# Performance work log

Measured on AMD Instinct MI355X. Metric: run time of the kernel, lower is better.

The kernel has to match this reference:

```python
import jax, jax.numpy as jnp
import numpy as np

DIM = 2048
HEADS = 16
HEAD_DIM = DIM // HEADS
B, S = 2, 2048


def setup_inputs() -> dict:
    key = jax.random.key(0)
    k1, k2, k3 = jax.random.split(key, 3)
    x = jax.random.normal(k1, (B, S, DIM), dtype=jnp.float32)
    # causal mask (True = keep), realistic production usage of masked_fill(mask==0,...)
    mask = jnp.tril(jnp.ones((S, S), dtype=bool))
    scale = 1.0 / np.sqrt(DIM)
    W_qkv = jax.random.normal(k2, (DIM, 3 * DIM), dtype=jnp.float32) * scale
    b_qkv = jnp.zeros((3 * DIM,), dtype=jnp.float32)
    W_out = jax.random.normal(k3, (DIM, DIM), dtype=jnp.float32) * scale
    b_out = jnp.zeros((DIM,), dtype=jnp.float32)
    return {"x": x, "mask": mask, "W_qkv": W_qkv, "b_qkv": b_qkv,
            "W_out": W_out, "b_out": b_out}


def reference(x, mask, W_qkv, b_qkv, W_out, b_out):
    b, s, d = x.shape
    # fused QKV projection: [b,s,3d]
    qkv = jnp.einsum('bsd,de->bse', x, W_qkv) + b_qkv
    # [b, s, h, 3*hd] -> [b, h, s, 3*hd] -> chunk into q,k,v
    qkv = qkv.reshape(b, s, HEADS, 3 * HEAD_DIM).transpose(0, 2, 1, 3)
    q, k, v = jnp.split(qkv, 3, axis=-1)  # each [b,h,s,hd]
    scores = jnp.einsum('bhqd,bhkd->bhqk', q, k) / np.sqrt(HEAD_DIM)
    scores = jnp.where(mask, scores, jnp.float32(-1e9))
    attn = jax.nn.softmax(scores, axis=-1)
    # dropout_rate = 0.0 (eval) -> identity
    out = jnp.einsum('bhqk,bhkd->bhqd', attn, v)  # [b,h,s,hd]
    out = out.transpose(0, 2, 1, 3).reshape(b, s, d)
    return jnp.einsum('bsd,de->bse', out, W_out) + b_out
```

## Files before the change

### kernel.cpp

```cpp
#include <hip/hip_runtime.h>
#include <hip/hip_bf16.h>

#define SEQ   2048
#define DIMSZ 2048
#define NHEAD 16
#define HD    128
#define KDIM  2048

typedef __attribute__((ext_vector_type(8))) short bf16x8;
typedef __attribute__((ext_vector_type(4))) float f32x4;
typedef __attribute__((ext_vector_type(4))) short short4v;
typedef __attribute__((ext_vector_type(4))) float float4v;

__device__ __forceinline__ short f2bf(float f) {
    union { __hip_bfloat16 h; short s; } u;
    u.h = __float2bfloat16(f);
    return u.s;
}

__device__ __forceinline__ unsigned pack_bf2(float lo, float hi) {
    return (unsigned)(unsigned short)f2bf(lo) | ((unsigned)(unsigned short)f2bf(hi) << 16);
}

__device__ __forceinline__ void gload_lds16(const void* g, void* l) {
    __builtin_amdgcn_global_load_lds(
        (const __attribute__((address_space(1))) void*)g,
        (__attribute__((address_space(3))) void*)l, 16, 0, 0);
}

__global__ __launch_bounds__(256) void cvt_bf16(const float* __restrict__ in,
                                                short* __restrict__ out) {
    int i = (blockIdx.x * 256 + threadIdx.x) * 4;
    float4v v = *reinterpret_cast<const float4v*>(in + i);
    short4v o;
    o[0] = f2bf(v[0]); o[1] = f2bf(v[1]); o[2] = f2bf(v[2]); o[3] = f2bf(v[3]);
    *reinterpret_cast<short4v*>(out + i) = o;
}

__global__ __launch_bounds__(256) void transpose_cvt(const float* __restrict__ in,
                                                     short* __restrict__ out,
                                                     int R, int C) {
    __shared__ float tile[32][33];
    int c0 = blockIdx.x * 32, r0 = blockIdx.y * 32;
    int tx = threadIdx.x, ty = threadIdx.y;
#pragma unroll
    for (int i = 0; i < 32; i += 8)
        tile[ty + i][tx] = in[(long)(r0 + ty + i) * C + c0 + tx];
    __syncthreads();
#pragma unroll
    for (int i = 0; i < 32; i += 8)
        out[(long)(c0 + ty + i) * R + r0 + tx] = f2bf(tile[tx][ty + i]);
}

template <int MODE, int BM, int BN, int WMC, int WNC>
__global__ __launch_bounds__(512, 2) void gemm8p(const short* __restrict__ A,
                                                 const short* __restrict__ Bt,
                                                 const float* __restrict__ bias,
                                                 float* __restrict__ outf,
                                                 short* __restrict__ q_buf,
                                                 short* __restrict__ k_buf,
                                                 short* __restrict__ vt_buf,
                                                 int ntx) {
    constexpr int QMW = (BM / 2) / WMC;
    constexpr int QNW = (BN / 2) / WNC;
    constexpr int MA = QMW / 16;
    constexpr int NB = QNW / 16;
    constexpr int UA = BM / 64, UB = BN / 64, UT = UA + UB;
    constexpr int BH0C = (BN / 2 + 63) / 64;
    constexpr int NE = UA / 2 + BH0C, NL = UT - NE;
    constexpr int S0 = 2, S2 = 2;
    constexpr int NT = KDIM / 64;

    __shared__ __align__(16) short Alds[2][BM * 64];
    __shared__ __align__(16) short Blds[2][BN * 64];

    const int tid = threadIdx.x;
    const int wv = tid >> 6, ln = tid & 63;
    const int lr = ln & 15, lg = ln >> 4;
    const int wm = wv / WNC, wn = wv % WNC;
    const int q8 = gridDim.x >> 3;
    const int id = blockIdx.x;
    const int swz = (id & 7) * q8 + (id >> 3);
    const int m0 = (swz / ntx) * BM, n0 = (swz % ntx) * BN;

    const int r_l = wv * 8 + (ln >> 3);
    const int g8 = ((ln & 7) ^ ((ln >> 3) & 7)) << 3;

#define STAGE_U(u, bufi, TT)                                                   \
    {                                                                          \
        const bool isA_ = (u) < UA / 2 || (u) >= UA / 2 + UB;                  \
        const int idx_ = (u) < UA / 2 ? (u)                                    \
                         : ((u) < UA / 2 + UB ? (u) - UA / 2 : (u) - UB);      \
        if (isA_)                                                              \
            gload_lds16(A + (long)(m0 + idx_ * 64 + r_l) * KDIM + (TT)*64 + g8,\
                        &Alds[bufi][idx_ * 4096 + wv * 512]);                  \
        else                                                                   \
            gload_lds16(Bt + (long)(n0 + idx_ * 64 + r_l) * KDIM + (TT)*64 + g8,\
                        &Blds[bufi][idx_ * 4096 + wv * 512]);                  \
    }

#define RD(L_, row_, kk_) \
    (*reinterpret_cast<const bf16x8*>(&(L_)[(row_)*64 + ((((kk_)*4 + lg) ^ ((row_)&7)) << 3)]))

#define RD_A(bufi, mh, bank)                                                   \
    _Pragma("unroll") for (int mi = 0; mi < MA; ++mi) {                        \
        int r_ = (mh) * (BM / 2) + wm * QMW + mi * 16 + lr;                    \
        bank[mi][0] = RD(Alds[bufi], r_, 0);                                   \
        bank[mi][1] = RD(Alds[bufi], r_, 1);                                   \
    }
#define RD_B(bufi, nh, bank)                                                   \
    _Pragma("unroll") for (int ni = 0; ni < NB; ++ni) {                        \
        int r_ = (nh) * (BN / 2) + wn * QNW + ni * 16 + lr;                    \
        bank[ni][0] = RD(Blds[bufi], r_, 0);                                   \
        bank[ni][1] = RD(Blds[bufi], r_, 1);                                   \
    }

#define MFMA_Q(qi, AB, BB)                                                     \
    __builtin_amdgcn_s_setprio(1);                                             \
    _Pragma("unroll") for (int kk = 0; kk < 2; ++kk)                           \
        _Pragma("unroll") for (int mi = 0; mi < MA; ++mi)                      \
            _Pragma("unroll") for (int ni = 0; ni < NB; ++ni)                  \
                acc[qi][mi][ni] = __builtin_amdgcn_mfma_f32_16x16x32_bf16(     \
                    AB[mi][kk], BB[ni][kk], acc[qi][mi][ni], 0, 0, 0);         \
    __builtin_amdgcn_s_setprio(0);

#define LGKM0()                                                                \
    asm volatile("s_waitcnt lgkmcnt(0)" ::: "memory");                         \
    __builtin_amdgcn_sched_barrier(0);
#define VMC(n) asm volatile("s_waitcnt vmcnt(%0)" ::"i"(n) : "memory");
#define BAR()                                                                  \
    __builtin_amdgcn_s_barrier();                                              \
    __builtin_amdgcn_sched_barrier(0);

    f32x4 acc[4][MA][NB] = {};
    bf16x8 aF0[MA][2], aF1[MA][2], bF0[NB][2], bF1[NB][2];

#pragma unroll
    for (int u = 0; u < UT; ++u) STAGE_U(u, 0, 0);
#pragma unroll
    for (int u = 0; u < NE; ++u) STAGE_U(u, 1, 1);
    VMC(NE);
    BAR();

#define TILE_BODY(PAR, T_)                                                     \
    {                                                                          \
        constexpr int cur = PAR, nxt = PAR ^ 1;                                \
                                      \
        RD_A(cur, 0, aF0);                                                     \
        RD_B(cur, 0, bF0);                                                     \
        if ((T_) + 1 < NT) {                                                   \
            STAGE_U(NE + 0, nxt, (T_) + 1);                                    \
            STAGE_U(NE + 1, nxt, (T_) + 1);                                    \
        }                                                                      \
        BAR();                                                                 \
        LGKM0();                                                               \
        MFMA_Q(0, aF0, bF0);                                                   \
        BAR();                                                                 \
                                        \
        RD_B(cur, 1, bF1);                                                     \
        if ((T_) + 1 < NT) {                                                   \
            _Pragma("unroll") for (int u = NE + S0; u < UT; ++u)               \
                STAGE_U(u, nxt, (T_) + 1);                                     \
        }                                                                      \
        BAR();                                                                 \
        LGKM0();                                                               \
        MFMA_Q(1, aF0, bF1);                                                   \
        BAR();                                                                 \
                                \
        RD_A(cur, 1, aF1);                                                     \
        if ((T_) + 2 < NT) {                                                   \
            STAGE_U(0, cur, (T_) + 2);                                         \
            STAGE_U(1, cur, (T_) + 2);                                         \
        }                                                                      \
        BAR();                                                                 \
        LGKM0();                                                               \
        MFMA_Q(2, aF1, bF1);                                                   \
        BAR();                                                                 \
          \
        if ((T_) + 2 < NT) {                                                   \
            _Pragma("unroll") for (int u = S2; u < NE; ++u)                    \
                STAGE_U(u, cur, (T_) + 2);                                     \
        }                                                                      \
        MFMA_Q(3, aF1, bF0);                                                   \
        if ((T_) + 2 < NT) { VMC(NE); } else { VMC(0); }                       \
        BAR();                                                                 \
    }

    for (int TT = 0; TT < NT; TT += 2) {
        TILE_BODY(0, TT);
        TILE_BODY(1, TT + 1);
    }

    const int MH[4] = {0, 0, 1, 1}, NHq[4] = {0, 1, 1, 0};
#pragma unroll
    for (int q = 0; q < 4; ++q) {
#pragma unroll
        for (int mi = 0; mi < MA; ++mi) {
#pragma unroll
            for (int ni = 0; ni < NB; ++ni) {
                int col = n0 + NHq[q] * (BN / 2) + wn * QNW + ni * 16 + lr;
                float bv = bias[col];
#pragma unroll
                for (int j = 0; j < 4; ++j) {
                    int row = m0 + MH[q] * (BM / 2) + wm * QMW + mi * 16 + lg * 4 + j;
                    float v = acc[q][mi][ni][j] + bv;
                    if (MODE == 0) {
                        int h = col / (3 * HD);
                        int jj = col - h * (3 * HD);
                        int b = row >> 11, s = row & 2047;
                        int bh = b * NHEAD + h;
                        short sv = f2bf(v);
                        if (jj < HD)
                            q_buf[(bh * SEQ + s) * HD + jj] = sv;
                        else if (jj < 2 * HD)
                            k_buf[(bh * SEQ + s) * HD + (jj - HD)] = sv;
                        else
                            vt_buf[(bh * HD + (jj - 2 * HD)) * SEQ + s] = sv;
                    } else {
                        outf[(long)row * DIMSZ + col] = v;
                    }
                }
            }
        }
    }
#undef STAGE_U
#undef RD
#undef RD_A
#undef RD_B
#undef MFMA_Q
#undef LGKM0
#undef VMC
#undef BAR
#undef TILE_BODY
}

__global__ __launch_bounds__(256, 2) void attn_kernel(const short* __restrict__ q_buf,
                                                      const short* __restrict__ k_buf,
                                                      const short* __restrict__ vt_buf,
                                                      short* __restrict__ ao) {
    __shared__ __align__(16) short Klds[2][64 * 128];
    __shared__ __align__(16) short Vlds[2][128 * 64];
    const int tid = threadIdx.x;
    const int wave = tid >> 6, lane = tid & 63;
    const int lr = lane & 15, lg = lane >> 4;
    const int bx = blockIdx.x;
    const int qt = 15 - (bx >> 5);
    const int bh = bx & 31;
    const int b = bh >> 4, h = bh & 15;
    const int qbase = qt * 128 + wave * 32;
    const float c2 = 0.12752775f;

    bf16x8 qf[2][4];
    {
        const short* qrow = q_buf + ((long)(bh * SEQ + qbase + lr)) * HD;
#pragma unroll
        for (int mi = 0; mi < 2; ++mi)
#pragma unroll
            for (int c = 0; c < 4; ++c)
                qf[mi][c] = *reinterpret_cast<const bf16x8*>(
                    qrow + mi * 16 * HD + c * 32 + lg * 8);
    }
    asm volatile("s_waitcnt vmcnt(0)" ::: "memory");

    const char* kbase = (const char*)(k_buf + (long)bh * SEQ * HD);
    const char* vbase = (const char*)(vt_buf + (long)bh * HD * SEQ);
    const int krow_l = wave * 4 + (lane >> 4);
    const int kcol_l = ((lane & 15) * 16) ^ ((krow_l & 7) << 4);
    const int vrow_l = wave * 8 + (lane >> 3);
    const int vcol_l = ((lane & 7) * 16) ^ ((vrow_l & 7) << 4);

    const int nt = 2 * (qt + 1);
    auto stage = [&](int bufi, int t) {
        const char* ks = kbase + (long)t * 16384 + (long)krow_l * 256 + kcol_l;
        const char* vs = vbase + (long)t * 128 + (long)vrow_l * (SEQ * 2) + vcol_l;
        short* kd = &Klds[bufi][wave * 512];
        short* vd = &Vlds[bufi][wave * 512];
#pragma unroll
        for (int i = 0; i < 4; ++i) {
            gload_lds16(ks + i * 4096, kd + i * 2048);
            gload_lds16(vs + (long)i * 32 * SEQ * 2, vd + i * 2048);
        }
    };

    f32x4 o_acc[2][8] = {};
    float mrow[2] = {-1e30f, -1e30f}, lrow[2] = {0.f, 0.f};

    const int s0 = (lane & 15) | ((lane & 16) << 1);
    const int s1 = s0 + 16;
    const bool hi_ni = (lane & 32) != 0;

    stage(0, 0);
    for (int t = 0; t < nt; ++t) {
        const int cur = t & 1;
        if (t + 1 < nt) {
            stage(cur ^ 1, t + 1);
            asm volatile("s_waitcnt vmcnt(8)" ::: "memory");
        } else {
            asm volatile("s_waitcnt vmcnt(0)" ::: "memory");
        }
        __builtin_amdgcn_s_barrier();
        __builtin_amdgcn_sched_barrier(0);

        const int kv0 = t * 64;
        if (kv0 <= qbase + 31) {
            f32x4 sc[2][4] = {};
            const short* kl = &Klds[cur][0];
#pragma unroll
            for (int c = 0; c < 4; ++c) {
                bf16x8 kf[4];
#pragma unroll
                for (int ni = 0; ni < 4; ++ni)
                    kf[ni] = *reinterpret_cast<const bf16x8*>(
                        kl + (((ni * 16 + lr) * 256 +
                               ((c * 64 + lg * 16) ^ ((lr & 7) << 4))) >> 1));
                __builtin_amdgcn_s_setprio(1);
#pragma unroll
                for (int mi = 0; mi < 2; ++mi)
#pragma unroll
                    for (int ni = 0; ni < 4; ++ni)
                        sc[mi][ni] = __builtin_amdgcn_mfma_f32_16x16x32_bf16(
                            kf[ni], qf[mi][c], sc[mi][ni], 0, 0, 0);
                __builtin_amdgcn_s_setprio(0);
            }
            const bool full = (kv0 + 63) <= qbase;
            float pv[2][4][4], mx[2];
#pragma unroll
            for (int mi = 0; mi < 2; ++mi) {
                float m_ = -3e38f;
                const int qg = qbase + mi * 16 + lr;
#pragma unroll
                for (int ni = 0; ni < 4; ++ni)
#pragma unroll
                    for (int j = 0; j < 4; ++j) {
                        float v = sc[mi][ni][j] * c2;
                        if (!full && (kv0 + ni * 16 + lg * 4 + j > qg)) v = -1e9f;
                        pv[mi][ni][j] = v;
                        m_ = fmaxf(m_, v);
                    }
                mx[mi] = m_;
            }
#pragma unroll
            for (int mi = 0; mi < 2; ++mi) {
                mx[mi] = fmaxf(mx[mi], __shfl_xor(mx[mi], 16, 64));
                mx[mi] = fmaxf(mx[mi], __shfl_xor(mx[mi], 32, 64));
            }
            float md = fmaxf(mx[0] - mrow[0], mx[1] - mrow[1]);
            if (!__all(md <= 11.5f)) {
#pragma unroll
                for (int mi = 0; mi < 2; ++mi) {
                    float mn = fmaxf(mrow[mi], mx[mi]);
                    float a = exp2f(mrow[mi] - mn);
                    mrow[mi] = mn;
                    lrow[mi] *= a;
#pragma unroll
                    for (int j = 0; j < 4; ++j) {
                        float aj = __shfl(a, (lane & 48) | (lg * 4 + j), 64);
#pragma unroll
                        for (int n = 0; n < 8; ++n)
                            o_acc[mi][n][j] *= aj;
                    }
                }
            }
            unsigned pk[2][4][2];
#pragma unroll
            for (int mi = 0; mi < 2; ++mi) {
                float ps = 0.f;
#pragma unroll
                for (int ni = 0; ni < 4; ++ni) {
#pragma unroll
                    for (int j = 0; j < 4; ++j) {
                        float p = exp2f(pv[mi][ni][j] - mrow[mi]);
                        pv[mi][ni][j] = p;
                        ps += p;
                    }
                    pk[mi][ni][0] = pack_bf2(pv[mi][ni][0], pv[mi][ni][1]);
                    pk[mi][ni][1] = pack_bf2(pv[mi][ni][2], pv[mi][ni][3]);
                }
                ps += __shfl_xor(ps, 16, 64);
                ps += __shfl_xor(ps, 32, 64);
                lrow[mi] += ps;
            }
            const short* vl = &Vlds[cur][0];
#pragma unroll
            for (int kc = 0; kc < 2; ++kc) {
                union { int i[4]; bf16x8 v; } pa[2];
#pragma unroll
                for (int mi = 0; mi < 2; ++mi) {
                    int a0 = __shfl((int)pk[mi][2 * kc][0], s0, 64);
                    int b0 = __shfl((int)pk[mi][2 * kc + 1][0], s0, 64);
                    int a1 = __shfl((int)pk[mi][2 * kc][1], s0, 64);
                    int b1 = __shfl((int)pk[mi][2 * kc + 1][1], s0, 64);
                    int a2 = __shfl((int)pk[mi][2 * kc][0], s1, 64);
                    int b2 = __shfl((int)pk[mi][2 * kc + 1][0], s1, 64);
                    int a3 = __shfl((int)pk[mi][2 * kc][1], s1, 64);
                    int b3 = __shfl((int)pk[mi][2 * kc + 1][1], s1, 64);
                    pa[mi].i[0] = hi_ni ? b0 : a0;
                    pa[mi].i[1] = hi_ni ? b1 : a1;
                    pa[mi].i[2] = hi_ni ? b2 : a2;
                    pa[mi].i[3] = hi_ni ? b3 : a3;
                }
#pragma unroll
                for (int n = 0; n < 8; ++n) {
                    bf16x8 vf = *reinterpret_cast<const bf16x8*>(
                        vl + (((n * 16 + lr) * 128 +
                               ((kc * 64 + lg * 16) ^ ((lr & 7) << 4))) >> 1));
                    __builtin_amdgcn_s_setprio(1);
#pragma unroll
                    for (int mi = 0; mi < 2; ++mi)
                        o_acc[mi][n] = __builtin_amdgcn_mfma_f32_16x16x32_bf16(
                            pa[mi].v, vf, o_acc[mi][n], 0, 0, 0);
                    __builtin_amdgcn_s_setprio(0);
                }
            }
        }
        __builtin_amdgcn_s_barrier();
    }

    float invq[2];
#pragma unroll
    for (int mi = 0; mi < 2; ++mi) invq[mi] = 1.0f / lrow[mi];
    short* aor = ao + ((long)(b * SEQ + qbase) * DIMSZ + h * HD);
#pragma unroll
    for (int mi = 0; mi < 2; ++mi)
#pragma unroll
        for (int j = 0; j < 4; ++j) {
            float ij = __shfl(invq[mi], (lane & 48) | (lg * 4 + j), 64);
#pragma unroll
            for (int n = 0; n < 8; ++n)
                aor[(mi * 16 + lg * 4 + j) * DIMSZ + n * 16 + lr] =
                    f2bf(o_acc[mi][n][j] * ij);
        }
}

extern "C" void kernel_launch(void* const* d_in, const int* in_sizes, int n_in,
                              void* d_out, int out_size, void* d_ws, size_t ws_size,
                              hipStream_t stream) {
    const float* x     = (const float*)d_in[0];
    const float* W_qkv = (const float*)d_in[2];
    const float* b_qkv = (const float*)d_in[3];
    const float* W_out = (const float*)d_in[4];
    const float* b_out = (const float*)d_in[5];
    float* out = (float*)d_out;

    char* ws = (char*)d_ws;
    short* x_bf   = (short*)ws;
    short* wqkv_t = (short*)(ws + (size_t)16 * 1048576);
    short* wout_t = (short*)(ws + (size_t)40 * 1048576);
    short* q_buf  = (short*)(ws + (size_t)48 * 1048576);
    short* k_buf  = (short*)(ws + (size_t)64 * 1048576);
    short* vt_buf = (short*)(ws + (size_t)80 * 1048576);
    short* ao     = x_bf;

    cvt_bf16<<<8192, 256, 0, stream>>>(x, x_bf);
    transpose_cvt<<<dim3(192, 64), dim3(32, 8), 0, stream>>>(W_qkv, wqkv_t, 2048, 6144);
    transpose_cvt<<<dim3(64, 64), dim3(32, 8), 0, stream>>>(W_out, wout_t, 2048, 2048);
    gemm8p<0, 256, 192, 4, 2><<<512, 512, 0, stream>>>(x_bf, wqkv_t, b_qkv, nullptr,
                                                       q_buf, k_buf, vt_buf, 32);
    attn_kernel<<<512, 256, 0, stream>>>(q_buf, k_buf, vt_buf, ao);
    gemm8p<1, 128, 256, 2, 4><<<256, 512, 0, stream>>>(ao, wout_t, b_out, out,
                                                       nullptr, nullptr, nullptr, 8);
}
```

Before: 298.2 us.

## Collapse GEMM main loop into a single read phase and back-to-back MFMA block

Replaces the four-phase interleaved schedule, with barriers and explicit lgkmcnt waits between each MFMA quadrant, with one phase per K tile. Each tile loads all A/B fragments from LDS up front, issues the next-tile global-to-LDS stages, runs all four MFMA quadrants back-to-back under raised priority, then stages the tile after next. This cuts barriers from about five to two per tile and removes the manual waits. In exchange it gives up the fine-grained overlap of LDS reads and MFMA, raises fragment register pressure, and leaves ordering of LDS reads to the compiler.

```diff
diff --git a/kernel.cpp b/kernel.cpp
--- a/kernel.cpp
+++ b/kernel.cpp
@@ -68,7 +68,6 @@
     constexpr int UA = BM / 64, UB = BN / 64, UT = UA + UB;
     constexpr int BH0C = (BN / 2 + 63) / 64;
     constexpr int NE = UA / 2 + BH0C, NL = UT - NE;
-    constexpr int S0 = 2, S2 = 2;
     constexpr int NT = KDIM / 64;
 
     __shared__ __align__(16) short Alds[2][BM * 64];
@@ -116,17 +115,12 @@
     }
 
 #define MFMA_Q(qi, AB, BB)                                                     \
-    __builtin_amdgcn_s_setprio(1);                                             \
     _Pragma("unroll") for (int kk = 0; kk < 2; ++kk)                           \
         _Pragma("unroll") for (int mi = 0; mi < MA; ++mi)                      \
             _Pragma("unroll") for (int ni = 0; ni < NB; ++ni)                  \
                 acc[qi][mi][ni] = __builtin_amdgcn_mfma_f32_16x16x32_bf16(     \
-                    AB[mi][kk], BB[ni][kk], acc[qi][mi][ni], 0, 0, 0);         \
-    __builtin_amdgcn_s_setprio(0);
-
-#define LGKM0()                                                                \
-    asm volatile("s_waitcnt lgkmcnt(0)" ::: "memory");                         \
-    __builtin_amdgcn_sched_barrier(0);
+                    AB[mi][kk], BB[ni][kk], acc[qi][mi][ni], 0, 0, 0);
+
 #define VMC(n) asm volatile("s_waitcnt vmcnt(%0)" ::"i"(n) : "memory");
 #define BAR()                                                                  \
     __builtin_amdgcn_s_barrier();                                              \
@@ -139,51 +133,32 @@
     for (int u = 0; u < UT; ++u) STAGE_U(u, 0, 0);
 #pragma unroll
     for (int u = 0; u < NE; ++u) STAGE_U(u, 1, 1);
-    VMC(NE);
-    BAR();
 
 #define TILE_BODY(PAR, T_)                                                     \
     {                                                                          \
         constexpr int cur = PAR, nxt = PAR ^ 1;                                \
-                                      \
+        if ((T_) + 1 < NT) { VMC(NE); } else { VMC(0); }                       \
+        BAR();                                                                 \
+                       \
         RD_A(cur, 0, aF0);                                                     \
         RD_B(cur, 0, bF0);                                                     \
+        RD_B(cur, 1, bF1);                                                     \
+        RD_A(cur, 1, aF1);                                                     \
         if ((T_) + 1 < NT) {                                                   \
-            STAGE_U(NE + 0, nxt, (T_) + 1);                                    \
-            STAGE_U(NE + 1, nxt, (T_) + 1);                                    \
-        }                                                                      \
-        BAR();                                                                 \
-        LGKM0();                                                               \
-        MFMA_Q(0, aF0, bF0);                                                   \
-        BAR();                                                                 \
-                                        \
-        RD_B(cur, 1, bF1);                                                     \
-        if ((T_) + 1 < NT) {                                                   \
-            _Pragma("unroll") for (int u = NE + S0; u < UT; ++u)               \
+            _Pragma("unroll") for (int u = NE; u < UT; ++u)                    \
                 STAGE_U(u, nxt, (T_) + 1);                                     \
         }                                                                      \
+        __builtin_amdgcn_s_setprio(1);                                         \
+        MFMA_Q(0, aF0, bF0);                                                   \
+        MFMA_Q(1, aF0, bF1);                                                   \
+        MFMA_Q(2, aF1, bF1);                                                   \
+        MFMA_Q(3, aF1, bF0);                                                   \
+        __builtin_amdgcn_s_setprio(0);                                         \
         BAR();                                                                 \
-        LGKM0();                                                               \
-        MFMA_Q(1, aF0, bF1);                                                   \
-        BAR();                                                                 \
-                                \
-        RD_A(cur, 1, aF1);                                                     \
         if ((T_) + 2 < NT) {                                                   \
-            STAGE_U(0, cur, (T_) + 2);                                         \
-            STAGE_U(1, cur, (T_) + 2);                                         \
-        }                                                                      \
-        BAR();                                                                 \
-        LGKM0();                                                               \
-        MFMA_Q(2, aF1, bF1);                                                   \
-        BAR();                                                                 \
-          \
-        if ((T_) + 2 < NT) {                                                   \
-            _Pragma("unroll") for (int u = S2; u < NE; ++u)                    \
+            _Pragma("unroll") for (int u = 0; u < NE; ++u)                     \
                 STAGE_U(u, cur, (T_) + 2);                                     \
         }                                                                      \
-        MFMA_Q(3, aF1, bF0);                                                   \
-        if ((T_) + 2 < NT) { VMC(NE); } else { VMC(0); }                       \
-        BAR();                                                                 \
     }
 
     for (int TT = 0; TT < NT; TT += 2) {
@@ -228,7 +203,6 @@
 #undef RD_A
 #undef RD_B
 #undef MFMA_Q
-#undef LGKM0
 #undef VMC
 #undef BAR
 #undef TILE_BODY
```

New measurement: 297.3 us. About the same (-0.3%).
